# Kernel optimization log

Measured on AMD Instinct MI355X. Metric: run time of the kernel, lower is better.

## Reference

```python
import jax, jax.numpy as jnp
import numpy as np

LATENT = 1024
HID = 512
J = 24
# SMPL kinematic tree (parent[0] = -1 is the root, unused in the loop)
PARENT = [-1, 0, 0, 0, 1, 2, 3, 4, 5, 6, 7, 8, 9, 9, 9, 12, 13, 14, 16, 17, 18, 19, 20, 21]
EPS = 1e-12  # F.normalize default eps


def setup_inputs() -> dict:
    key = jax.random.key(0)
    k1, k2, k3, k4, k5 = jax.random.split(key, 5)
    B = 32768
    # Kaiming-uniform-ish init scales for the Linear layers
    s1 = 1.0 / np.sqrt(LATENT)
    s2 = 1.0 / np.sqrt(HID)
    return {
        "z": jax.random.normal(k1, (B, LATENT), dtype=jnp.float32),
        "W1": jax.random.uniform(k2, (LATENT, HID), minval=-s1, maxval=s1, dtype=jnp.float32),
        "b1": jax.random.uniform(k3, (HID,), minval=-s1, maxval=s1, dtype=jnp.float32),
        "W2": jax.random.uniform(k4, (HID, (J - 1) * 4), minval=-s2, maxval=s2, dtype=jnp.float32),
        "b2": jax.random.uniform(k5, ((J - 1) * 4,), minval=-s2, maxval=s2, dtype=jnp.float32),
    }


def reference(z, W1, b1, W2, b2):
    B = z.shape[0]
    h = jax.nn.silu(z @ W1 + b1)                    # [B, 512]
    raw = (h @ W2 + b2).reshape(B, J - 1, 4)        # [B, J-1, 4]
    vec = raw[..., :3]                              # [B, J-1, 3]
    norm = jnp.linalg.norm(vec, axis=-1, keepdims=True)
    direction = vec / jnp.maximum(norm, EPS)        # F.normalize(dim=-1)
    length = jax.nn.softplus(raw[..., 3])           # [B, J-1]
    child_off = direction * length[..., None]       # [B, J-1, 3]
    offsets = jnp.concatenate(
        [jnp.zeros((B, 1, 3), dtype=z.dtype), child_off], axis=1
    )                                                # [B, J, 3]
    # Static-tree forward kinematics: unroll the (small, fixed) joint loop.
    joints_list = [jnp.zeros((B, 3), dtype=z.dtype)]
    for j in range(1, J):
        joints_list.append(joints_list[PARENT[j]] + offsets[:, j])
    joints = jnp.stack(joints_list, axis=1)          # [B, J, 3]
    return (joints, offsets, length)
```

## Files before the change

kernel.cpp:

```cpp
#include <hip/hip_runtime.h>
#include <hip/hip_bf16.h>
#include <stdint.h>

#define BROWS 32768
#define LATENT 1024
#define HID 512

typedef float f32x4 __attribute__((ext_vector_type(4)));
typedef __bf16 bf16x8 __attribute__((ext_vector_type(8)));
typedef unsigned short us8 __attribute__((ext_vector_type(8)));

__device__ __forceinline__ void gload16(const void* g, void* l) {
  __builtin_amdgcn_global_load_lds(
      (__attribute__((address_space(1))) void*)g,
      (__attribute__((address_space(3))) void*)l, 16, 0, 0);
}

__device__ __forceinline__ void split_bf16(float x, unsigned short& hi, unsigned short& lo) {
  __bf16 h = (__bf16)x;
  float r = x - (float)h;
  __bf16 l = (__bf16)r;
  hi = __builtin_bit_cast(unsigned short, h);
  lo = __builtin_bit_cast(unsigned short, l);
}

__device__ __forceinline__ f32x4 mfma16(bf16x8 a, bf16x8 b, f32x4 c) {
  return __builtin_amdgcn_mfma_f32_16x16x32_bf16(a, b, c, 0, 0, 0);
}

__device__ __forceinline__ bf16x8 ldfrag(const void* p) {
  return __builtin_bit_cast(bf16x8, *(const us8*)p);
}

__global__ __launch_bounds__(256) void k_prep_w1f(const float* __restrict__ W1,
                                                  unsigned short* __restrict__ w1f) {
  const int n = blockIdx.x;
  const int t = threadIdx.x;
  const int kt = t >> 3, ls = t & 7;
  const int p = ls ^ (n & 7);
  const int k0 = kt * 32 + (ls & 3) * 8;
  unsigned short v[8];
#pragma unroll
  for (int e = 0; e < 8; e++) {
    const float x = W1[(size_t)(k0 + e) * HID + n];
    unsigned short h, q;
    split_bf16(x, h, q);
    v[e] = (ls < 4) ? h : q;
  }
  unsigned short* dst = w1f + ((size_t)n * 32 + kt) * 64 + p * 8;
  *(ushort4*)(dst) = make_ushort4(v[0], v[1], v[2], v[3]);
  *(ushort4*)(dst + 4) = make_ushort4(v[4], v[5], v[6], v[7]);
}

__global__ __launch_bounds__(256) void k_prep_w2t(const float* __restrict__ W2,
                                                  unsigned short* __restrict__ hi,
                                                  unsigned short* __restrict__ lo) {
  const int idx = blockIdx.x * 256 + threadIdx.x;
  const int n = idx >> 9, k = idx & 511;
  const float v = (n < 92) ? W2[(size_t)k * 92 + n] : 0.0f;
  unsigned short h, l;
  split_bf16(v, h, l);
  hi[idx] = h;
  lo[idx] = l;
}

__global__ __launch_bounds__(512, 2) void k_gemm1(
    const float* __restrict__ z, const unsigned short* __restrict__ w1f,
    const float* __restrict__ b1,
    unsigned short* __restrict__ hh, unsigned short* __restrict__ hl) {
  extern __shared__ __align__(16) char lb[];

  const int tid = threadIdx.x;
  const int bid = blockIdx.x;
  const int swzb = (bid & 7) * 32 + (bid >> 3);
  const int mb = swzb >> 1, nbk = swzb & 1;
  const int m0 = mb * 256, n0g = nbk * 256;

  const int wv = tid >> 6, l = tid & 63;
  const int wr = wv >> 2, wc = wv & 3;
  const int l15 = l & 15, lg = l >> 4;
  const int xr = l15 & 7;

  const int ahB = (wr * 128 + l15) * 128 + ((lg ^ xr) << 4);
  const int alB = (wr * 128 + l15) * 128 + ((((4 | lg) ^ xr)) << 4);
  const int bhB = 32768 + (wc * 64 + l15) * 128 + ((lg ^ xr) << 4);
  const int blB = 32768 + (wc * 64 + l15) * 128 + ((((4 | lg) ^ xr)) << 4);

  const int arow = tid >> 3;
  const int kc4 = tid & 7;
  const int xw = arow & 7;
  const int hi_off = (((kc4 >> 1) ^ xw) << 4) + (kc4 & 1) * 8;
  const int lo_off = ((((4 | (kc4 >> 1)) ^ xw)) << 4) + (kc4 & 1) * 8;
  const float* zb = z + (size_t)(m0 + arow) * LATENT + kc4 * 4;

  const unsigned short* bsrc =
      w1f + ((size_t)(n0g + wv * 32 + (l >> 3)) * 32) * 64 + (l & 7) * 8;

  f32x4 acc[8][4] = {};
  float4 zr[4];

#define LOAD_ZR(kt1)                                                          \
  {                                                                           \
    _Pragma("unroll") for (int i_ = 0; i_ < 4; i_++)                          \
        zr[i_] = *(const float4*)(zb + (size_t)(64 * i_) * LATENT + (kt1) * 32); \
  }

#define WRITE_A(bufo)                                                         \
  {                                                                           \
    _Pragma("unroll") for (int i_ = 0; i_ < 4; i_++) {                        \
      unsigned short h0, h1, h2, h3, q0, q1, q2, q3;                          \
      split_bf16(zr[i_].x, h0, q0); split_bf16(zr[i_].y, h1, q1);             \
      split_bf16(zr[i_].z, h2, q2); split_bf16(zr[i_].w, h3, q3);             \
      char* rp = lb + (bufo) + (arow + 64 * i_) * 128;                        \
      *(ushort4*)(rp + hi_off) = make_ushort4(h0, h1, h2, h3);                \
      *(ushort4*)(rp + lo_off) = make_ushort4(q0, q1, q2, q3);                \
    }                                                                         \
  }

#define GLOAD_B(bufo, kt1)                                                    \
  {                                                                           \
    _Pragma("unroll") for (int j_ = 0; j_ < 4; j_++)                          \
        gload16(bsrc + (size_t)j_ * 16384 + (kt1) * 64,                       \
                lb + (bufo) + 32768 + (wv * 32 + j_ * 8) * 128);              \
  }

#define MCLUSTER(AF, BF)                                                      \
  {                                                                           \
    __builtin_amdgcn_s_setprio(1);                                            \
    _Pragma("unroll") for (int mf = 0; mf < 8; mf++)                          \
        _Pragma("unroll") for (int nf = 0; nf < 4; nf++)                      \
            acc[mf][nf] = mfma16(AF[mf], BF[nf], acc[mf][nf]);                \
    __builtin_amdgcn_s_setprio(0);                                            \
  }

  GLOAD_B(0, 0);
  LOAD_ZR(0);
  asm volatile("s_waitcnt vmcnt(0)" ::: "memory");
  WRITE_A(0);
  LOAD_ZR(1);
  asm volatile("s_waitcnt lgkmcnt(0)" ::: "memory");
  __builtin_amdgcn_s_barrier();
  __builtin_amdgcn_sched_barrier(0);

#pragma unroll 2
  for (int t = 0; t < 32; ++t) {
    const int cb = (t & 1) * 65536;
    const int nb2 = cb ^ 65536;

    bf16x8 ah[8], bh[4];
#pragma unroll
    for (int mf = 0; mf < 8; mf++) ah[mf] = ldfrag(lb + cb + ahB + mf * 2048);
#pragma unroll
    for (int nf = 0; nf < 4; nf++) bh[nf] = ldfrag(lb + cb + bhB + nf * 2048);

    if (t < 31) {
      WRITE_A(nb2);
      GLOAD_B(nb2, t + 1);
      asm volatile("" ::: "memory");
      if (t < 30) LOAD_ZR(t + 2);
    }

    MCLUSTER(ah, bh);

    {
      bf16x8 alf[8];
#pragma unroll
      for (int mf = 0; mf < 8; mf++) alf[mf] = ldfrag(lb + cb + alB + mf * 2048);
      MCLUSTER(alf, bh);
    }

    {
      bf16x8 blf[4];
#pragma unroll
      for (int nf = 0; nf < 4; nf++) blf[nf] = ldfrag(lb + cb + blB + nf * 2048);
      MCLUSTER(ah, blf);
    }

    if (t < 30) { asm volatile("s_waitcnt vmcnt(4)" ::: "memory"); }
    else        { asm volatile("s_waitcnt vmcnt(0)" ::: "memory"); }
    asm volatile("s_waitcnt lgkmcnt(0)" ::: "memory");
    __builtin_amdgcn_s_barrier();
    __builtin_amdgcn_sched_barrier(0);
  }

  float b1v[4];
#pragma unroll
  for (int nf = 0; nf < 4; nf++) b1v[nf] = b1[n0g + wc * 64 + nf * 16 + l15];

#pragma unroll
  for (int mf = 0; mf < 8; mf++)
#pragma unroll
    for (int nf = 0; nf < 4; nf++)
#pragma unroll
      for (int r = 0; r < 4; r++) {
        const int gm = m0 + wr * 128 + mf * 16 + (lg << 2) + r;
        const int gn = n0g + wc * 64 + nf * 16 + l15;
        const float x = acc[mf][nf][r] + b1v[nf];
        const float hval = x / (1.0f + expf(-x));
        unsigned short hi_, lo_;
        split_bf16(hval, hi_, lo_);
        const size_t o = (size_t)gm * HID + gn;
        hh[o] = hi_;
        hl[o] = lo_;
      }
}

__global__ __launch_bounds__(256, 2) void k_gemm2(
    const unsigned short* __restrict__ hh, const unsigned short* __restrict__ hl,
    const unsigned short* __restrict__ w2h, const unsigned short* __restrict__ w2l,
    const float* __restrict__ b2, float* __restrict__ out) {
  __shared__ unsigned short Ah[2][2048], Al[2][2048];
  __shared__ unsigned short Bh[2][4096], Bl[2][4096];
  __shared__ float raw[64][97];

  const int tid = threadIdx.x;
  const int m0 = blockIdx.x * 64;
  const int w = tid >> 6, lane = tid & 63;
  const int wr = w >> 1, wc = w & 1;
  const int l15 = lane & 15, lg = lane >> 4;
  const int arow = tid >> 2, ac8 = (tid & 3) << 3;

  const unsigned short* hhb = hh + (size_t)(m0 + arow) * HID + ac8;
  const unsigned short* hlb = hl + (size_t)(m0 + arow) * HID + ac8;
  const unsigned short* w2hb = w2h + (size_t)arow * HID + ac8;
  const unsigned short* w2lb = w2l + (size_t)arow * HID + ac8;

  f32x4 acc[2][3] = {};

#define G2_STAGE(kt, bf) { \
    gload16(hhb + (kt) * 32, &Ah[bf][(w << 9)]); \
    gload16(hlb + (kt) * 32, &Al[bf][(w << 9)]); \
    gload16(w2hb + (kt) * 32,            &Bh[bf][(w << 9)]); \
    gload16(w2hb + (kt) * 32 + 64 * HID, &Bh[bf][2048 + (w << 9)]); \
    gload16(w2lb + (kt) * 32,            &Bl[bf][(w << 9)]); \
    gload16(w2lb + (kt) * 32 + 64 * HID, &Bl[bf][2048 + (w << 9)]); }

#define G2_COMPUTE(bf) { \
    bf16x8 ah2[2], al2[2], bh2[3], bl2[3]; \
    _Pragma("unroll") \
    for (int mf = 0; mf < 2; mf++) { \
      const int o_ = ((wr * 32 + mf * 16 + l15) << 5) + (lg << 3); \
      ah2[mf] = ldfrag(&Ah[bf][o_]); \
      al2[mf] = ldfrag(&Al[bf][o_]); \
    } \
    _Pragma("unroll") \
    for (int nf = 0; nf < 3; nf++) { \
      const int o_ = ((wc * 48 + nf * 16 + l15) << 5) + (lg << 3); \
      bh2[nf] = ldfrag(&Bh[bf][o_]); \
      bl2[nf] = ldfrag(&Bl[bf][o_]); \
    } \
    _Pragma("unroll") \
    for (int mf = 0; mf < 2; mf++) { \
      _Pragma("unroll") \
      for (int nf = 0; nf < 3; nf++) { \
        acc[mf][nf] = mfma16(ah2[mf], bh2[nf], acc[mf][nf]); \
        acc[mf][nf] = mfma16(al2[mf], bh2[nf], acc[mf][nf]); \
        acc[mf][nf] = mfma16(ah2[mf], bl2[nf], acc[mf][nf]); \
      } } }

  G2_STAGE(0, 0);
  __syncthreads();
#pragma unroll 2
  for (int kt = 0; kt < 16; kt++) {
    const int cur = kt & 1, nx = cur ^ 1;
    if (kt < 15) G2_STAGE(kt + 1, nx);
    G2_COMPUTE(cur);
    __syncthreads();
  }

#pragma unroll
  for (int mf = 0; mf < 2; mf++) {
#pragma unroll
    for (int nf = 0; nf < 3; nf++) {
#pragma unroll
      for (int r = 0; r < 4; r++) {
        const int ml = wr * 32 + mf * 16 + (lg << 2) + r;
        const int nl = wc * 48 + nf * 16 + l15;
        raw[ml][nl] = acc[mf][nf][r];
      }
    }
  }
  __syncthreads();

  const size_t OFFB = (size_t)BROWS * 72;
  const size_t LENB = (size_t)BROWS * 144;

  for (int task = tid; task < 64 * 24; task += 256) {
    const int row = task / 24;
    const int j = task - row * 24;
    const int gm = m0 + row;
    float* orow = out + OFFB + (size_t)gm * 72;
    if (j == 0) {
      orow[0] = 0.0f; orow[1] = 0.0f; orow[2] = 0.0f;
    } else {
      const int c0 = (j - 1) * 4;
      const float vx = raw[row][c0 + 0] + b2[c0 + 0];
      const float vy = raw[row][c0 + 1] + b2[c0 + 1];
      const float vz = raw[row][c0 + 2] + b2[c0 + 2];
      const float wvv = raw[row][c0 + 3] + b2[c0 + 3];
      const float nrm = sqrtf(vx * vx + vy * vy + vz * vz);
      const float inv = 1.0f / fmaxf(nrm, 1e-12f);
      const float len = fmaxf(wvv, 0.0f) + log1pf(expf(-fabsf(wvv)));
      const float sc = inv * len;
      const float ox = vx * sc, oy = vy * sc, oz = vz * sc;
      orow[j * 3 + 0] = ox; orow[j * 3 + 1] = oy; orow[j * 3 + 2] = oz;
      out[LENB + (size_t)gm * 23 + (j - 1)] = len;
      raw[row][c0 + 0] = ox; raw[row][c0 + 1] = oy; raw[row][c0 + 2] = oz;
    }
  }
  __syncthreads();

  if (tid < 64) {
    constexpr int PAR[24] = {-1, 0, 0, 0, 1, 2, 3, 4, 5, 6, 7, 8,
                             9, 9, 9, 12, 13, 14, 16, 17, 18, 19, 20, 21};
    const int gm = m0 + tid;
    float e[72];
    e[0] = 0.0f; e[1] = 0.0f; e[2] = 0.0f;
#pragma unroll
    for (int j = 1; j < 24; j++) {
      const int p = PAR[j];
      const int c0 = (j - 1) * 4;
      e[3 * j + 0] = e[3 * p + 0] + raw[tid][c0 + 0];
      e[3 * j + 1] = e[3 * p + 1] + raw[tid][c0 + 1];
      e[3 * j + 2] = e[3 * p + 2] + raw[tid][c0 + 2];
    }
    float4* jo = (float4*)(out + (size_t)gm * 72);
#pragma unroll
    for (int q = 0; q < 18; q++)
      jo[q] = make_float4(e[4 * q + 0], e[4 * q + 1], e[4 * q + 2], e[4 * q + 3]);
  }
}

extern "C" void kernel_launch(void* const* d_in, const int* in_sizes, int n_in,
                              void* d_out, int out_size, void* d_ws, size_t ws_size,
                              hipStream_t stream) {
  const float* z = (const float*)d_in[0];
  const float* W1 = (const float*)d_in[1];
  const float* b1 = (const float*)d_in[2];
  const float* W2 = (const float*)d_in[3];
  const float* b2 = (const float*)d_in[4];
  float* out = (float*)d_out;

  char* ws = (char*)d_ws;
  unsigned short* w1f = (unsigned short*)(ws);
  unsigned short* w2h = (unsigned short*)(ws + (2 << 20));
  unsigned short* w2l = (unsigned short*)(ws + (2 << 20) + 131072);
  unsigned short* hh = (unsigned short*)(ws + ((size_t)4 << 20));
  unsigned short* hl = (unsigned short*)(ws + ((size_t)4 << 20) + ((size_t)32 << 20));

  static bool attr_set = false;
  (void)attr_set;
  hipFuncSetAttribute((const void*)k_gemm1,
                      hipFuncAttributeMaxDynamicSharedMemorySize, 131072);

  hipLaunchKernelGGL(k_prep_w1f, dim3(512), dim3(256), 0, stream, W1, w1f);
  hipLaunchKernelGGL(k_prep_w2t, dim3(256), dim3(256), 0, stream, W2, w2h, w2l);
  hipLaunchKernelGGL(k_gemm1, dim3(256), dim3(512), 131072, stream, z, w1f, b1, hh, hl);
  hipLaunchKernelGGL(k_gemm2, dim3(512), dim3(256), 0, stream, hh, hl, w2h, w2l, b2, out);
}
```

Before: 151.1 us.

## Load z directly into MFMA A-fragments in registers, shrink gemm1 tile to 128x256

k_gemm1 no longer stages z through LDS. Each wave loads fp32 z straight from global memory into registers in the MFMA A-fragment layout and splits it into bf16 hi/lo there, so only W1 tiles are double-buffered in LDS via global_load_lds. The block tile drops from 256x256 with 512 threads to 128x256 with 256 threads, using 64 KB of LDS and a 512-block grid. This is meant to cut LDS write and read traffic and barrier cost and to allow more blocks per CU, at the cost of redundant global z reads across waves (wc=0/1 both load the same rows) and less B reuse per block.

```diff
diff --git a/kernel.cpp b/kernel.cpp
--- a/kernel.cpp
+++ b/kernel.cpp
@@ -64,7 +64,7 @@
   lo[idx] = l;
 }
 
-__global__ __launch_bounds__(512, 2) void k_gemm1(
+__global__ __launch_bounds__(256, 2) void k_gemm1(
     const float* __restrict__ z, const unsigned short* __restrict__ w1f,
     const float* __restrict__ b1,
     unsigned short* __restrict__ hh, unsigned short* __restrict__ hl) {
@@ -72,129 +72,108 @@
 
   const int tid = threadIdx.x;
   const int bid = blockIdx.x;
-  const int swzb = (bid & 7) * 32 + (bid >> 3);
-  const int mb = swzb >> 1, nbk = swzb & 1;
-  const int m0 = mb * 256, n0g = nbk * 256;
+  const int swz = (bid & 7) * 64 + (bid >> 3);
+  const int mb = swz >> 1, nbk = swz & 1;
+  const int m0 = mb * 128, n0g = nbk * 256;
 
   const int wv = tid >> 6, l = tid & 63;
-  const int wr = wv >> 2, wc = wv & 3;
+  const int wr = wv >> 1, wc = wv & 1;
   const int l15 = l & 15, lg = l >> 4;
   const int xr = l15 & 7;
 
-  const int ahB = (wr * 128 + l15) * 128 + ((lg ^ xr) << 4);
-  const int alB = (wr * 128 + l15) * 128 + ((((4 | lg) ^ xr)) << 4);
-  const int bhB = 32768 + (wc * 64 + l15) * 128 + ((lg ^ xr) << 4);
-  const int blB = 32768 + (wc * 64 + l15) * 128 + ((((4 | lg) ^ xr)) << 4);
-
-  const int arow = tid >> 3;
-  const int kc4 = tid & 7;
-  const int xw = arow & 7;
-  const int hi_off = (((kc4 >> 1) ^ xw) << 4) + (kc4 & 1) * 8;
-  const int lo_off = ((((4 | (kc4 >> 1)) ^ xw)) << 4) + (kc4 & 1) * 8;
-  const float* zb = z + (size_t)(m0 + arow) * LATENT + kc4 * 4;
+  const int bhB = (wc * 128 + l15) * 128 + ((lg ^ xr) << 4);
+  const int blB = (wc * 128 + l15) * 128 + ((((4 | lg) ^ xr)) << 4);
+
+  const float* zb = z + (size_t)(m0 + wr * 64 + l15) * LATENT + lg * 8;
 
   const unsigned short* bsrc =
-      w1f + ((size_t)(n0g + wv * 32 + (l >> 3)) * 32) * 64 + (l & 7) * 8;
-
-  f32x4 acc[8][4] = {};
-  float4 zr[4];
-
-#define LOAD_ZR(kt1)                                                          \
+      w1f + ((size_t)(n0g + wv * 64 + (l >> 3)) * 32) * 64 + (l & 7) * 8;
+
+  f32x4 acc[4][8] = {};
+  float4 arl[4], arh[4];
+  bf16x8 ah[4], alo[4];
+
+#define LOAD_A(kt1)                                                           \
   {                                                                           \
-    _Pragma("unroll") for (int i_ = 0; i_ < 4; i_++)                          \
-        zr[i_] = *(const float4*)(zb + (size_t)(64 * i_) * LATENT + (kt1) * 32); \
-  }
-
-#define WRITE_A(bufo)                                                         \
+    _Pragma("unroll") for (int mf = 0; mf < 4; mf++) {                        \
+      const float* p_ = zb + (size_t)(16 * mf) * LATENT + (kt1) * 32;         \
+      arl[mf] = *(const float4*)(p_);                                         \
+      arh[mf] = *(const float4*)(p_ + 4);                                     \
+    }                                                                         \
+  }
+
+#define SPLIT_A                                                               \
   {                                                                           \
-    _Pragma("unroll") for (int i_ = 0; i_ < 4; i_++) {                        \
-      unsigned short h0, h1, h2, h3, q0, q1, q2, q3;                          \
-      split_bf16(zr[i_].x, h0, q0); split_bf16(zr[i_].y, h1, q1);             \
-      split_bf16(zr[i_].z, h2, q2); split_bf16(zr[i_].w, h3, q3);             \
-      char* rp = lb + (bufo) + (arow + 64 * i_) * 128;                        \
-      *(ushort4*)(rp + hi_off) = make_ushort4(h0, h1, h2, h3);                \
-      *(ushort4*)(rp + lo_off) = make_ushort4(q0, q1, q2, q3);                \
+    _Pragma("unroll") for (int mf = 0; mf < 4; mf++) {                        \
+      _Pragma("unroll") for (int e = 0; e < 4; e++) {                         \
+        float f0 = arl[mf][e], f1 = arh[mf][e];                               \
+        __bf16 h0 = (__bf16)f0, h1 = (__bf16)f1;                              \
+        ah[mf][e] = h0;     alo[mf][e] = (__bf16)(f0 - (float)h0);            \
+        ah[mf][4 + e] = h1; alo[mf][4 + e] = (__bf16)(f1 - (float)h1);        \
+      }                                                                       \
     }                                                                         \
   }
 
 #define GLOAD_B(bufo, kt1)                                                    \
   {                                                                           \
-    _Pragma("unroll") for (int j_ = 0; j_ < 4; j_++)                          \
+    _Pragma("unroll") for (int j_ = 0; j_ < 8; j_++)                          \
         gload16(bsrc + (size_t)j_ * 16384 + (kt1) * 64,                       \
-                lb + (bufo) + 32768 + (wv * 32 + j_ * 8) * 128);              \
-  }
-
-#define MCLUSTER(AF, BF)                                                      \
+                lb + (bufo) + (wv * 64 + j_ * 8) * 128);                      \
+  }
+
+#define COMPUTE(bufo)                                                         \
   {                                                                           \
     __builtin_amdgcn_s_setprio(1);                                            \
-    _Pragma("unroll") for (int mf = 0; mf < 8; mf++)                          \
-        _Pragma("unroll") for (int nf = 0; nf < 4; nf++)                      \
-            acc[mf][nf] = mfma16(AF[mf], BF[nf], acc[mf][nf]);                \
+    _Pragma("unroll") for (int nf = 0; nf < 8; nf++) {                        \
+      bf16x8 bh = ldfrag(lb + (bufo) + bhB + nf * 2048);                      \
+      _Pragma("unroll") for (int mf = 0; mf < 4; mf++)                        \
+          acc[mf][nf] = mfma16(ah[mf], bh, acc[mf][nf]);                      \
+      _Pragma("unroll") for (int mf = 0; mf < 4; mf++)                        \
+          acc[mf][nf] = mfma16(alo[mf], bh, acc[mf][nf]);                     \
+    }                                                                         \
+    _Pragma("unroll") for (int nf = 0; nf < 8; nf++) {                        \
+      bf16x8 bl = ldfrag(lb + (bufo) + blB + nf * 2048);                      \
+      _Pragma("unroll") for (int mf = 0; mf < 4; mf++)                        \
+          acc[mf][nf] = mfma16(ah[mf], bl, acc[mf][nf]);                      \
+    }                                                                         \
     __builtin_amdgcn_s_setprio(0);                                            \
   }
 
   GLOAD_B(0, 0);
-  LOAD_ZR(0);
-  asm volatile("s_waitcnt vmcnt(0)" ::: "memory");
-  WRITE_A(0);
-  LOAD_ZR(1);
-  asm volatile("s_waitcnt lgkmcnt(0)" ::: "memory");
-  __builtin_amdgcn_s_barrier();
-  __builtin_amdgcn_sched_barrier(0);
+  LOAD_A(0);
 
 #pragma unroll 2
   for (int t = 0; t < 32; ++t) {
-    const int cb = (t & 1) * 65536;
-    const int nb2 = cb ^ 65536;
-
-    bf16x8 ah[8], bh[4];
-#pragma unroll
-    for (int mf = 0; mf < 8; mf++) ah[mf] = ldfrag(lb + cb + ahB + mf * 2048);
-#pragma unroll
-    for (int nf = 0; nf < 4; nf++) bh[nf] = ldfrag(lb + cb + bhB + nf * 2048);
+    const int cb = (t & 1) * 32768;
+    const int nb2 = cb ^ 32768;
+
+    asm volatile("s_waitcnt vmcnt(8)" ::: "memory");
+    __builtin_amdgcn_s_barrier();
 
     if (t < 31) {
-      WRITE_A(nb2);
       GLOAD_B(nb2, t + 1);
-      asm volatile("" ::: "memory");
-      if (t < 30) LOAD_ZR(t + 2);
+      asm volatile("s_waitcnt vmcnt(8)" ::: "memory");
+    } else {
+      asm volatile("s_waitcnt vmcnt(0)" ::: "memory");
     }
-
-    MCLUSTER(ah, bh);
-
-    {
-      bf16x8 alf[8];
-#pragma unroll
-      for (int mf = 0; mf < 8; mf++) alf[mf] = ldfrag(lb + cb + alB + mf * 2048);
-      MCLUSTER(alf, bh);
-    }
-
-    {
-      bf16x8 blf[4];
-#pragma unroll
-      for (int nf = 0; nf < 4; nf++) blf[nf] = ldfrag(lb + cb + blB + nf * 2048);
-      MCLUSTER(ah, blf);
-    }
-
-    if (t < 30) { asm volatile("s_waitcnt vmcnt(4)" ::: "memory"); }
-    else        { asm volatile("s_waitcnt vmcnt(0)" ::: "memory"); }
-    asm volatile("s_waitcnt lgkmcnt(0)" ::: "memory");
-    __builtin_amdgcn_s_barrier();
-    __builtin_amdgcn_sched_barrier(0);
-  }
-
-  float b1v[4];
-#pragma unroll
-  for (int nf = 0; nf < 4; nf++) b1v[nf] = b1[n0g + wc * 64 + nf * 16 + l15];
-
-#pragma unroll
-  for (int mf = 0; mf < 8; mf++)
-#pragma unroll
-    for (int nf = 0; nf < 4; nf++)
+    SPLIT_A;
+    if (t < 31) LOAD_A(t + 1);
+
+    COMPUTE(cb);
+  }
+
+  float b1v[8];
+#pragma unroll
+  for (int nf = 0; nf < 8; nf++) b1v[nf] = b1[n0g + wc * 128 + nf * 16 + l15];
+
+#pragma unroll
+  for (int mf = 0; mf < 4; mf++)
+#pragma unroll
+    for (int nf = 0; nf < 8; nf++)
 #pragma unroll
       for (int r = 0; r < 4; r++) {
-        const int gm = m0 + wr * 128 + mf * 16 + (lg << 2) + r;
-        const int gn = n0g + wc * 64 + nf * 16 + l15;
+        const int gm = m0 + wr * 64 + mf * 16 + (lg << 2) + r;
+        const int gn = n0g + wc * 128 + nf * 16 + l15;
         const float x = acc[mf][nf][r] + b1v[nf];
         const float hval = x / (1.0f + expf(-x));
         unsigned short hi_, lo_;
@@ -348,13 +327,11 @@
   unsigned short* hh = (unsigned short*)(ws + ((size_t)4 << 20));
   unsigned short* hl = (unsigned short*)(ws + ((size_t)4 << 20) + ((size_t)32 << 20));
 
-  static bool attr_set = false;
-  (void)attr_set;
   hipFuncSetAttribute((const void*)k_gemm1,
                       hipFuncAttributeMaxDynamicSharedMemorySize, 131072);
 
   hipLaunchKernelGGL(k_prep_w1f, dim3(512), dim3(256), 0, stream, W1, w1f);
   hipLaunchKernelGGL(k_prep_w2t, dim3(256), dim3(256), 0, stream, W2, w2h, w2l);
-  hipLaunchKernelGGL(k_gemm1, dim3(256), dim3(512), 131072, stream, z, w1f, b1, hh, hl);
+  hipLaunchKernelGGL(k_gemm1, dim3(512), dim3(256), 65536, stream, z, w1f, b1, hh, hl);
   hipLaunchKernelGGL(k_gemm2, dim3(512), dim3(256), 0, stream, hh, hl, w2h, w2l, b2, out);
 }
```

After: 147.8 us. 2.2% less time.
